# Optimization experiments

Hardware: AMD Instinct MI355X
Metric: run time of the kernel (lower is better)

## Reference

```python
import jax, jax.numpy as jnp
import numpy as np

DIM = 512
HEADS = 8
DIM_HEAD = 64
INNER = HEADS * DIM_HEAD  # 512
HIDDEN = 512 * 4          # mlp_dim * expansion
EPS = 1e-5
SCALE = DIM_HEAD ** -0.5


def layernorm(x, w, b):
    mu = jnp.mean(x, axis=-1, keepdims=True)
    var = jnp.var(x, axis=-1, keepdims=True)
    return (x - mu) * jax.lax.rsqrt(var + EPS) * w + b


def setup_inputs() -> dict:
    key = jax.random.key(0)
    ks = jax.random.split(key, 12)
    B, P, N = 2, 8, 1024  # P must equal HEADS (axis-swap bug in original rearrange)
    s = lambda k, shape, fan: jax.random.normal(k, shape, jnp.float32) * (fan ** -0.5)
    return {
        "x": jax.random.normal(ks[0], (B, P, N, DIM), jnp.float32),
        "ln0_w": jnp.ones((DIM,), jnp.float32),
        "ln0_b": jnp.zeros((DIM,), jnp.float32),
        "ln1_w": jnp.ones((DIM,), jnp.float32),
        "ln1_b": jnp.zeros((DIM,), jnp.float32),
        "w_qkv": s(ks[1], (DIM, 3 * INNER), DIM),
        "w_o": s(ks[2], (INNER, DIM), INNER),
        "b_o": jnp.zeros((DIM,), jnp.float32),
        "w1": s(ks[3], (DIM, HIDDEN), DIM),
        "b1": jnp.zeros((HIDDEN,), jnp.float32),
        "w2": s(ks[4], (HIDDEN, DIM), HIDDEN),
        "b2": jnp.zeros((DIM,), jnp.float32),
    }


def reference(x, ln0_w, ln0_b, ln1_w, ln1_b, w_qkv, w_o, b_o, w1, b1, w2, b2):
    B, P, N, _ = x.shape
    x = layernorm(x, ln0_w, ln0_b)  # outer block norm

    # ---- VisionAttention ----
    h = layernorm(x, ln1_w, ln1_b)
    qkv = h @ w_qkv                                    # [B,P,N,3*INNER]
    q, k, v = jnp.split(qkv, 3, axis=-1)
    def to_heads(t):  # [B,P,N,H*D] -> [B,H,P,N,D]
        return t.reshape(B, P, N, HEADS, DIM_HEAD).transpose(0, 3, 1, 2, 4)
    q, k, v = to_heads(q), to_heads(k), to_heads(v)
    dots = jnp.einsum("bhpnd,bhpmd->bhpnm", q, k) * SCALE  # full NxN scores
    attn = jax.nn.softmax(dots, axis=-1)
    out = jnp.einsum("bhpnm,bhpmd->bhpnd", attn, v)        # [B,H,P,N,D]
    # Faithful to buggy rearrange 'b p h n d -> b p n (h d)': swaps H and P axes.
    out = out.transpose(0, 1, 3, 2, 4).reshape(B, HEADS, N, P * DIM_HEAD)
    out = out @ w_o + b_o                                  # [B,H,N,DIM]
    x = out + x  # residual (valid because P == HEADS)

    # ---- MLP ----
    m = jax.nn.gelu(x @ w1 + b1, approximate=False) @ w2 + b2
    return m + x
```

## Files before the change

### kernel.cpp

```cpp
#include <hip/hip_runtime.h>
#include <hip/hip_bf16.h>
#include <math.h>

#define DIMV 512
#define NTOK 16384
#define NSEQ 1024
#define HEADSV 8
#define PPV 8
#define DHEAD 64
#define QKVW 1536
#define HIDV 2048
#define SC2 0.18033688011112042f

typedef unsigned short ushort;
typedef unsigned int uint;
typedef __attribute__((ext_vector_type(8))) short short8;
typedef __attribute__((ext_vector_type(8))) unsigned short ushort8;
typedef __attribute__((ext_vector_type(4))) unsigned short ushortx4;
typedef __attribute__((ext_vector_type(4))) float floatx4;

__device__ __forceinline__ float bf2f(ushort u){
  union { unsigned int i; float f; } c; c.i = ((unsigned int)u) << 16; return c.f;
}
__device__ __forceinline__ ushort f2bf(float f){
  union { float f; unsigned int i; } c; c.f = f;
  unsigned int u = c.i + 0x7fffu + ((c.i >> 16) & 1u);
  return (ushort)(u >> 16);
}
__device__ __forceinline__ void async_copy16(const void* gptr, void* lptr){
  __builtin_amdgcn_global_load_lds((const __attribute__((address_space(1))) void*)gptr,
                                   (__attribute__((address_space(3))) void*)lptr, 16, 0, 0);
}
__device__ __forceinline__ float fast_gelu(float x){
  float u = x * (2.3022084f + 0.1029435f * x * x);
  return x * __builtin_amdgcn_rcpf(1.f + exp2f(-u));
}

__device__ __forceinline__ void wave_reduce2(float& a, float& b){
  #pragma unroll
  for (int off = 32; off > 0; off >>= 1){
    a += __shfl_down(a, off, 64);
    b += __shfl_down(b, off, 64);
  }
}

__device__ __forceinline__ void wtrans_body(const float* __restrict__ W,
    __hip_bfloat16* __restrict__ Wt, int K, int N, int bx, int by, int t,
    float* tile ){
  int bn = bx * 32, bk = by * 32;
  int tx = t & 31, ty = t >> 5;
  #pragma unroll
  for (int i = 0; i < 32; i += 8)
    tile[(ty + i) * 33 + tx] = W[(size_t)(bk + ty + i) * N + bn + tx];
  __syncthreads();
  #pragma unroll
  for (int i = 0; i < 32; i += 8)
    Wt[(size_t)(bn + ty + i) * K + bk + tx] = __float2bfloat16(tile[tx * 33 + ty + i]);
}

__global__ __launch_bounds__(256) void prep_kernel(const float* __restrict__ x,
    const float* __restrict__ w0, const float* __restrict__ b0,
    const float* __restrict__ w1ln, const float* __restrict__ b1ln,
    __hip_bfloat16* __restrict__ x1, __hip_bfloat16* __restrict__ h,
    const float* __restrict__ wqkv, __hip_bfloat16* __restrict__ wqkvT,
    const float* __restrict__ wo,   __hip_bfloat16* __restrict__ woT,
    const float* __restrict__ w1,   __hip_bfloat16* __restrict__ w1T,
    const float* __restrict__ w2,   __hip_bfloat16* __restrict__ w2T){
  __shared__ float smem[32 * 33];
  int bid = blockIdx.x;
  int t = threadIdx.x;
  if (bid >= NTOK){
    int r = bid - NTOK;
    if (r < 768)        wtrans_body(wqkv, wqkvT, 512, 1536, r % 48, r / 48, t, smem);
    else if (r < 1024){ r -= 768;  wtrans_body(wo, woT, 512, 512,  r % 16, r / 16, t, smem); }
    else if (r < 2048){ r -= 1024; wtrans_body(w1, w1T, 512, 2048, r % 64, r / 64, t, smem); }
    else             { r -= 2048; wtrans_body(w2, w2T, 2048, 512, r % 16, r / 16, t, smem); }
    return;
  }
  float* sm = smem;
  size_t row = bid;
  const float2* xr = (const float2*)(x + row * DIMV);
  float2 v = xr[t];
  float s = v.x + v.y;
  float sq = v.x * v.x + v.y * v.y;
  wave_reduce2(s, sq);
  int wid = t >> 6, lane = t & 63;
  if (lane == 0){ sm[wid] = s; sm[8 + wid] = sq; }
  __syncthreads();
  s  = sm[0] + sm[1] + sm[2] + sm[3];
  sq = sm[8] + sm[9] + sm[10] + sm[11];
  float mu = s * (1.f / DIMV);
  float var = sq * (1.f / DIMV) - mu * mu;
  float r = rsqrtf(var + 1e-5f);
  float2 ww = ((const float2*)w0)[t];
  float2 bb = ((const float2*)b0)[t];
  float2 y;
  y.x = (v.x - mu) * r * ww.x + bb.x;
  y.y = (v.y - mu) * r * ww.y + bb.y;
  ushort2 xb; xb.x = f2bf(y.x); xb.y = f2bf(y.y);
  ((ushort2*)(x1 + row * DIMV))[t] = xb;
  float s2 = y.x + y.y, sq2 = y.x * y.x + y.y * y.y;
  wave_reduce2(s2, sq2);
  __syncthreads();
  if (lane == 0){ sm[wid] = s2; sm[8 + wid] = sq2; }
  __syncthreads();
  s2  = sm[0] + sm[1] + sm[2] + sm[3];
  sq2 = sm[8] + sm[9] + sm[10] + sm[11];
  float mu2 = s2 * (1.f / DIMV);
  float var2 = sq2 * (1.f / DIMV) - mu2 * mu2;
  float r2 = rsqrtf(var2 + 1e-5f);
  float2 w1v = ((const float2*)w1ln)[t];
  float2 b1v = ((const float2*)b1ln)[t];
  float hx = (y.x - mu2) * r2 * w1v.x + b1v.x;
  float hy = (y.y - mu2) * r2 * w1v.y + b1v.y;
  ushort2 hb; hb.x = f2bf(hx); hb.y = f2bf(hy);
  ((ushort2*)(h + row * DIMV))[t] = hb;
}

template<int SWAP>
__global__ __launch_bounds__(256) void gemm_mfma(
    const __hip_bfloat16* __restrict__ A,
    const __hip_bfloat16* __restrict__ Bt,
    const float* __restrict__ bias,
    const __hip_bfloat16* __restrict__ Rb,
    float* __restrict__ Cf,
    __hip_bfloat16* __restrict__ Cb,
    ushort* __restrict__ vt,
    int M, int N, int K, int gx, int dogelu)
{
  __shared__ __hip_bfloat16 As[2][128 * 32];
  __shared__ __hip_bfloat16 Bs[2][128 * 32];
  int tid = threadIdx.x;
  int w = tid >> 6, l = tid & 63;

  int bid = blockIdx.x;
  int xcd = bid & 7, idx = bid >> 3;
  int xl = idx % gx, yl = idx / gx;
  size_t bm = (size_t)(xcd * 16 + yl) * 128;
  size_t bn = (size_t)xl * 128;
  int wm = (w & 1) * 64, wn = (w >> 1) * 64;

  int srow = w * 16 + (l >> 2);
  int scol = (l & 3) * 8;
  const __hip_bfloat16* Ag0 = A + (bm + srow) * K + scol;
  const __hip_bfloat16* Ag1 = A + (bm + 64 + srow) * K + scol;
  const __hip_bfloat16* Bg0 = Bt + (bn + srow) * K + scol;
  const __hip_bfloat16* Bg1 = Bt + (bn + 64 + srow) * K + scol;
  int lo = srow * 32 + scol;

  floatx4 acc[4][4] = {};
  int fm = l & 15;
  int quad = l >> 4;
  int fq = quad * 8;

  async_copy16(Ag0, &As[0][lo]);
  async_copy16(Ag1, &As[0][lo + 64 * 32]);
  async_copy16(Bg0, &Bs[0][lo]);
  async_copy16(Bg1, &Bs[0][lo + 64 * 32]);

  int nk = K >> 5;
  for (int it = 0; it < nk; ++it){
    int cur = it & 1;
    if (it + 1 < nk){
      int nxt = cur ^ 1;
      int k0 = (it + 1) << 5;
      async_copy16(Ag0 + k0, &As[nxt][lo]);
      async_copy16(Ag1 + k0, &As[nxt][lo + 64 * 32]);
      async_copy16(Bg0 + k0, &Bs[nxt][lo]);
      async_copy16(Bg1 + k0, &Bs[nxt][lo + 64 * 32]);
      asm volatile("s_waitcnt vmcnt(4)\n\ts_barrier" ::: "memory");
    } else {
      asm volatile("s_waitcnt vmcnt(0)\n\ts_barrier" ::: "memory");
    }
    const __hip_bfloat16* Ab = As[cur];
    const __hip_bfloat16* Bb = Bs[cur];
    short8 af[4], bf[4];
    #pragma unroll
    for (int i = 0; i < 4; i++){
      af[i] = *(const short8*)&Ab[(wm + i * 16 + fm) * 32 + fq];
      bf[i] = *(const short8*)&Bb[(wn + i * 16 + fm) * 32 + fq];
    }
    #pragma unroll
    for (int mi = 0; mi < 4; mi++)
      #pragma unroll
      for (int ni = 0; ni < 4; ni++){
        if (SWAP)
          acc[mi][ni] = __builtin_amdgcn_mfma_f32_16x16x32_bf16(bf[ni], af[mi], acc[mi][ni], 0, 0, 0);
        else
          acc[mi][ni] = __builtin_amdgcn_mfma_f32_16x16x32_bf16(af[mi], bf[ni], acc[mi][ni], 0, 0, 0);
      }
    asm volatile("s_waitcnt lgkmcnt(0)\n\ts_barrier" ::: "memory");
  }

  int rq = quad * 4;
  if (SWAP){
    #pragma unroll
    for (int mi = 0; mi < 4; mi++){
      size_t row = bm + wm + mi * 16 + fm;
      size_t rbase = row * (size_t)N + bn + wn + rq;
      #pragma unroll
      for (int ni = 0; ni < 4; ni++){
        size_t idx2 = rbase + ni * 16;
        floatx4 v = acc[mi][ni];
        if (bias){
          floatx4 bv = *(const floatx4*)(bias + bn + wn + ni * 16 + rq);
          #pragma unroll
          for (int r2 = 0; r2 < 4; r2++) v[r2] += bv[r2];
        }
        if (dogelu){
          #pragma unroll
          for (int r2 = 0; r2 < 4; r2++) v[r2] = fast_gelu(v[r2]);
        }
        if (Rb){
          ushortx4 rb = *(const ushortx4*)((const ushort*)Rb + idx2);
          #pragma unroll
          for (int r2 = 0; r2 < 4; r2++) v[r2] += bf2f(rb[r2]);
        }
        if (Cb){
          ushortx4 ob;
          #pragma unroll
          for (int r2 = 0; r2 < 4; r2++) ob[r2] = f2bf(v[r2]);
          *(ushortx4*)((ushort*)Cb + idx2) = ob;
        } else {
          *(floatx4*)(Cf + idx2) = v;
        }
      }
    }
  } else {
    if (vt && bn >= 1024){
      int b = (int)(bm >> 13), p = (int)((bm >> 10) & 7);
      int n0 = (int)(bm & 1023) + wm + rq;
      int cbase = (int)bn + wn - 1024;
      #pragma unroll
      for (int ni = 0; ni < 4; ni++){
        int cc = cbase + ni * 16 + fm;
        int hh = cc >> 6, dd = cc & 63;
        ushort* vdst = vt + ((size_t)((b * 8 + hh) * 8 + p)) * 65536 + (size_t)dd * 1024;
        #pragma unroll
        for (int mi = 0; mi < 4; mi++){
          ushortx4 v4;
          v4[0] = f2bf(acc[mi][ni][0]); v4[1] = f2bf(acc[mi][ni][1]);
          v4[2] = f2bf(acc[mi][ni][2]); v4[3] = f2bf(acc[mi][ni][3]);
          *(ushortx4*)(vdst + n0 + mi * 16) = v4;
        }
      }
    } else if (Cb){
      float scl = (vt && bn < 512) ? SC2 : 1.f;
      #pragma unroll
      for (int ni = 0; ni < 4; ni++){
        size_t col = bn + wn + ni * 16 + fm;
        float bv = bias ? bias[col] : 0.f;
        #pragma unroll
        for (int mi = 0; mi < 4; mi++){
          #pragma unroll
          for (int r2 = 0; r2 < 4; r2++){
            size_t row = bm + wm + mi * 16 + rq + r2;
            float v = acc[mi][ni][r2];
            if (vt) v *= scl;
            v += bv;
            if (dogelu) v = fast_gelu(v);
            size_t idx2 = row * N + col;
            if (Rb) v += bf2f(((const ushort*)Rb)[idx2]);
            ((ushort*)Cb)[idx2] = f2bf(v);
          }
        }
      }
    } else {
      #pragma unroll
      for (int ni = 0; ni < 4; ni++){
        size_t col = bn + wn + ni * 16 + fm;
        float bv = bias ? bias[col] : 0.f;
        #pragma unroll
        for (int mi = 0; mi < 4; mi++){
          #pragma unroll
          for (int r2 = 0; r2 < 4; r2++){
            size_t row = bm + wm + mi * 16 + rq + r2;
            float v = acc[mi][ni][r2] + bv;
            if (dogelu) v = fast_gelu(v);
            size_t idx2 = row * N + col;
            if (Rb) v += bf2f(((const ushort*)Rb)[idx2]);
            Cf[idx2] = v;
          }
        }
      }
    }
  }
}

__global__ __launch_bounds__(256, 4) void attn_mfma(const __hip_bfloat16* __restrict__ qkvp,
                                                    const ushort* __restrict__ vt,
                                                    __hip_bfloat16* __restrict__ outp){
  __shared__ ushort Ks[2][64 * 64];
  __shared__ ushort Ps[4][32 * 64];
  int tid = threadIdx.x;
  int w = tid >> 6, l = tid & 63;
  int r15 = l & 15, quad = l >> 4, fq = quad * 8;
  int slice = blockIdx.x & 127;
  int qc = blockIdx.x >> 7;
  int b = slice >> 6, hh = (slice >> 3) & 7, p = slice & 7;
  const ushort* base = (const ushort*)qkvp + (size_t)(b * PPV + p) * NSEQ * QKVW;
  const ushort* kb = base + 512 + hh * DHEAD;
  const ushort* vb = vt + (size_t)slice * 65536;

  int s0 = w * 64 + l, s1 = 256 + w * 64 + l;
  int row0 = s0 >> 3, row1 = s1 >> 3;
  int gc0 = (s0 & 7) ^ (row0 & 7), gc1 = (s1 & 7) ^ (row1 & 7);
  const ushort* kp0 = kb + (size_t)row0 * QKVW + gc0 * 8;
  const ushort* kp1 = kb + (size_t)row1 * QKVW + gc1 * 8;
  ushort* kd0 = &Ks[0][s0 * 8];
  ushort* kd1 = &Ks[0][s1 * 8];

  const ushort* vr[4];
  #pragma unroll
  for (int dj = 0; dj < 4; dj++)
    vr[dj] = vb + (size_t)(dj * 16 + r15) * 1024 + fq;

  int q0 = qc * 128 + w * 32;
  short8 qf[2][2];
  #pragma unroll
  for (int mi = 0; mi < 2; mi++)
    #pragma unroll
    for (int kk = 0; kk < 2; kk++)
      qf[mi][kk] = *(const short8*)(base + (size_t)(q0 + mi * 16 + r15) * QKVW + hh * DHEAD + kk * 32 + fq);

  async_copy16(kp0, kd0);
  async_copy16(kp1, kd1);

  floatx4 o[2][4] = {};
  floatx4 lacc[2] = {};
  short8 ones;
  #pragma unroll
  for (int j = 0; j < 8; j++) ones[j] = (short)0x3F80;

  int sw = r15 & 7;
  int swx = sw << 3;
  ushort* PsW = Ps[w];

  for (int it = 0; it < NSEQ / 64; ++it){
    int cur = it & 1;
    short8 vf[4][2];
    #pragma unroll
    for (int dj = 0; dj < 4; dj++){
      vf[dj][0] = *(const short8*)(vr[dj]);
      vf[dj][1] = *(const short8*)(vr[dj] + 32);
      vr[dj] += 64;
    }
    if (it + 1 < NSEQ / 64){
      int nxt = cur ^ 1;
      kp0 += 64 * QKVW; kp1 += 64 * QKVW;
      async_copy16(kp0, &Ks[nxt][s0 * 8]);
      async_copy16(kp1, &Ks[nxt][s1 * 8]);
      asm volatile("s_waitcnt vmcnt(10)\n\ts_barrier" ::: "memory");
    } else {
      asm volatile("s_waitcnt vmcnt(8)\n\ts_barrier" ::: "memory");
    }
    const ushort* Kb = Ks[cur];

    #pragma unroll
    for (int ni = 0; ni < 4; ni++){
      int rb2 = (ni * 16 + r15) * 64;
      short8 kf0 = *(const short8*)&Kb[rb2 + (quad ^ sw) * 8];
      short8 kf1 = *(const short8*)&Kb[rb2 + ((4 + quad) ^ sw) * 8];
      floatx4 sA = {}, sB = {};
      sA = __builtin_amdgcn_mfma_f32_16x16x32_bf16(kf0, qf[0][0], sA, 0, 0, 0);
      sA = __builtin_amdgcn_mfma_f32_16x16x32_bf16(kf1, qf[0][1], sA, 0, 0, 0);
      sB = __builtin_amdgcn_mfma_f32_16x16x32_bf16(kf0, qf[1][0], sB, 0, 0, 0);
      sB = __builtin_amdgcn_mfma_f32_16x16x32_bf16(kf1, qf[1][1], sB, 0, 0, 0);
      int wc = (ni * 16 + quad * 4) ^ swx;
      #pragma unroll
      for (int mi = 0; mi < 2; mi++){
        const floatx4& sv = mi ? sB : sA;
        union { float f; uint u; } e0, e1, e2, e3;
        e0.f = exp2f(sv[0]);
        e1.f = exp2f(sv[1]);
        e2.f = exp2f(sv[2]);
        e3.f = exp2f(sv[3]);
        uint2 pk;
        pk.x = __builtin_amdgcn_perm(e1.u, e0.u, 0x07060302u);
        pk.y = __builtin_amdgcn_perm(e3.u, e2.u, 0x07060302u);
        *(uint2*)&PsW[(mi * 16 + r15) * 64 + wc] = pk;
      }
    }

    short8 pf[2][2];
    #pragma unroll
    for (int mi = 0; mi < 2; mi++)
      #pragma unroll
      for (int kk = 0; kk < 2; kk++)
        pf[mi][kk] = *(const short8*)&PsW[(mi * 16 + r15) * 64 + ((kk * 32 + fq) ^ swx)];

    #pragma unroll
    for (int mi = 0; mi < 2; mi++)
      #pragma unroll
      for (int kk = 0; kk < 2; kk++)
        lacc[mi] = __builtin_amdgcn_mfma_f32_16x16x32_bf16(ones, pf[mi][kk], lacc[mi], 0, 0, 0);

    #pragma unroll
    for (int dj = 0; dj < 4; dj++){
      #pragma unroll
      for (int mi = 0; mi < 2; mi++){
        o[mi][dj] = __builtin_amdgcn_mfma_f32_16x16x32_bf16(vf[dj][0], pf[mi][0], o[mi][dj], 0, 0, 0);
        o[mi][dj] = __builtin_amdgcn_mfma_f32_16x16x32_bf16(vf[dj][1], pf[mi][1], o[mi][dj], 0, 0, 0);
      }
    }
    asm volatile("s_waitcnt lgkmcnt(0)\n\ts_barrier" ::: "memory");
  }

  #pragma unroll
  for (int mi = 0; mi < 2; mi++){
    float inv = __builtin_amdgcn_rcpf(lacc[mi][0]);
    size_t n = q0 + mi * 16 + r15;
    ushort* orow = (ushort*)outp + ((size_t)((b * HEADSV + hh) * NSEQ + n)) * DIMV + p * DHEAD + quad * 4;
    #pragma unroll
    for (int dj = 0; dj < 4; dj++){
      ushortx4 ov;
      #pragma unroll
      for (int r = 0; r < 4; r++) ov[r] = f2bf(o[mi][dj][r] * inv);
      *(ushortx4*)(orow + dj * 16) = ov;
    }
  }
}

extern "C" void kernel_launch(void* const* d_in, const int* in_sizes, int n_in,
                              void* d_out, int out_size, void* d_ws, size_t ws_size,
                              hipStream_t stream){
  (void)in_sizes; (void)n_in; (void)out_size; (void)ws_size;
  const float* x    = (const float*)d_in[0];
  const float* lw0  = (const float*)d_in[1];
  const float* lb0  = (const float*)d_in[2];
  const float* lw1  = (const float*)d_in[3];
  const float* lb1  = (const float*)d_in[4];
  const float* wqkv = (const float*)d_in[5];
  const float* wo   = (const float*)d_in[6];
  const float* bo   = (const float*)d_in[7];
  const float* w1   = (const float*)d_in[8];
  const float* b1   = (const float*)d_in[9];
  const float* w2   = (const float*)d_in[10];
  const float* b2   = (const float*)d_in[11];
  float* out = (float*)d_out;
  char* ws = (char*)d_ws;
  const size_t MB = 1024 * 1024;

  __hip_bfloat16* x1b  = (__hip_bfloat16*)(ws);
  ushort* vtbuf        = (ushort*)(ws + 32 * MB);
  __hip_bfloat16* x2b  = (__hip_bfloat16*)(ws + 64 * MB);
  __hip_bfloat16* wqkvT= (__hip_bfloat16*)(ws + 80 * MB);
  __hip_bfloat16* woT  = (__hip_bfloat16*)(ws + 82 * MB);
  __hip_bfloat16* w1T  = (__hip_bfloat16*)(ws + 83 * MB);
  __hip_bfloat16* w2T  = (__hip_bfloat16*)(ws + 85 * MB);
  __hip_bfloat16* hB   = (__hip_bfloat16*)(ws + 88 * MB);
  __hip_bfloat16* attnB= hB;
  __hip_bfloat16* qkvB = (__hip_bfloat16*)(ws + 104 * MB);
  __hip_bfloat16* tB   = (__hip_bfloat16*)(ws + 88 * MB);

  prep_kernel<<<NTOK + 3072, 256, 0, stream>>>(
      x, lw0, lb0, lw1, lb1, x1b, hB,
      wqkv, wqkvT, wo, woT, w1, w1T, w2, w2T);

  gemm_mfma<0><<<(QKVW / 128) * 128, 256, 0, stream>>>(
      hB, wqkvT, nullptr, nullptr, nullptr, qkvB, vtbuf,
      NTOK, QKVW, DIMV, QKVW / 128, 0);

  attn_mfma<<<1024, 256, 0, stream>>>(qkvB, vtbuf, attnB);

  gemm_mfma<1><<<(DIMV / 128) * 128, 256, 0, stream>>>(
      attnB, woT, bo, x1b, nullptr, x2b, nullptr,
      NTOK, DIMV, DIMV, DIMV / 128, 0);

  gemm_mfma<1><<<(HIDV / 128) * 128, 256, 0, stream>>>(
      x2b, w1T, b1, nullptr, nullptr, tB, nullptr,
      NTOK, HIDV, DIMV, HIDV / 128, 1);

  gemm_mfma<1><<<(DIMV / 128) * 128, 256, 0, stream>>>(
      tB, w2T, b2, x2b, out, nullptr, nullptr,
      NTOK, DIMV, HIDV, DIMV / 128, 0);
}
```

Measured before the change: 386.8 us.

## Stage V tiles through double-buffered LDS and halve the P scratch buffer

V fragments used to be loaded per thread straight from global memory. They are now copied asynchronously into a double-buffered LDS tile next to K and read back with the swizzled pattern. The score loop is split into two 32-column halves, so each wave's P scratch shrinks to 32x32 and each half is read back before the next one is written. This removes scattered global V loads and cuts P LDS usage, at the cost of more LDS for V and extra lgkmcnt waits inside the loop.

```diff
diff --git a/kernel.cpp b/kernel.cpp
--- a/kernel.cpp
+++ b/kernel.cpp
@@ -291,7 +291,8 @@
                                                     const ushort* __restrict__ vt,
                                                     __hip_bfloat16* __restrict__ outp){
   __shared__ ushort Ks[2][64 * 64];
-  __shared__ ushort Ps[4][32 * 64];
+  __shared__ ushort Vs[2][64 * 64];
+  __shared__ ushort Ps[4][32 * 32];
   int tid = threadIdx.x;
   int w = tid >> 6, l = tid & 63;
   int r15 = l & 15, quad = l >> 4, fq = quad * 8;
@@ -307,13 +308,13 @@
   int gc0 = (s0 & 7) ^ (row0 & 7), gc1 = (s1 & 7) ^ (row1 & 7);
   const ushort* kp0 = kb + (size_t)row0 * QKVW + gc0 * 8;
   const ushort* kp1 = kb + (size_t)row1 * QKVW + gc1 * 8;
-  ushort* kd0 = &Ks[0][s0 * 8];
-  ushort* kd1 = &Ks[0][s1 * 8];
-
-  const ushort* vr[4];
-  #pragma unroll
-  for (int dj = 0; dj < 4; dj++)
-    vr[dj] = vb + (size_t)(dj * 16 + r15) * 1024 + fq;
+  const ushort* vp0 = vb + (size_t)row0 * 1024 + gc0 * 8;
+  const ushort* vp1 = vb + (size_t)row1 * 1024 + gc1 * 8;
+
+  async_copy16(kp0, &Ks[0][s0 * 8]);
+  async_copy16(kp1, &Ks[0][s1 * 8]);
+  async_copy16(vp0, &Vs[0][s0 * 8]);
+  async_copy16(vp1, &Vs[0][s1 * 8]);
 
   int q0 = qc * 128 + w * 32;
   short8 qf[2][2];
@@ -322,9 +323,6 @@
     #pragma unroll
     for (int kk = 0; kk < 2; kk++)
       qf[mi][kk] = *(const short8*)(base + (size_t)(q0 + mi * 16 + r15) * QKVW + hh * DHEAD + kk * 32 + fq);
-
-  async_copy16(kp0, kd0);
-  async_copy16(kp1, kd1);
 
   floatx4 o[2][4] = {};
   floatx4 lacc[2] = {};
@@ -333,61 +331,58 @@
   for (int j = 0; j < 8; j++) ones[j] = (short)0x3F80;
 
   int sw = r15 & 7;
-  int swx = sw << 3;
+  int swp = (r15 & 3) << 3;
   ushort* PsW = Ps[w];
 
   for (int it = 0; it < NSEQ / 64; ++it){
     int cur = it & 1;
-    short8 vf[4][2];
-    #pragma unroll
-    for (int dj = 0; dj < 4; dj++){
-      vf[dj][0] = *(const short8*)(vr[dj]);
-      vf[dj][1] = *(const short8*)(vr[dj] + 32);
-      vr[dj] += 64;
-    }
     if (it + 1 < NSEQ / 64){
       int nxt = cur ^ 1;
-      kp0 += 64 * QKVW; kp1 += 64 * QKVW;
+      kp0 += 64 * QKVW; kp1 += 64 * QKVW; vp0 += 64; vp1 += 64;
       async_copy16(kp0, &Ks[nxt][s0 * 8]);
       async_copy16(kp1, &Ks[nxt][s1 * 8]);
-      asm volatile("s_waitcnt vmcnt(10)\n\ts_barrier" ::: "memory");
+      async_copy16(vp0, &Vs[nxt][s0 * 8]);
+      async_copy16(vp1, &Vs[nxt][s1 * 8]);
+      asm volatile("s_waitcnt vmcnt(4)\n\ts_barrier" ::: "memory");
     } else {
-      asm volatile("s_waitcnt vmcnt(8)\n\ts_barrier" ::: "memory");
+      asm volatile("s_waitcnt vmcnt(0)\n\ts_barrier" ::: "memory");
     }
     const ushort* Kb = Ks[cur];
-
-    #pragma unroll
-    for (int ni = 0; ni < 4; ni++){
-      int rb2 = (ni * 16 + r15) * 64;
-      short8 kf0 = *(const short8*)&Kb[rb2 + (quad ^ sw) * 8];
-      short8 kf1 = *(const short8*)&Kb[rb2 + ((4 + quad) ^ sw) * 8];
-      floatx4 sA = {}, sB = {};
-      sA = __builtin_amdgcn_mfma_f32_16x16x32_bf16(kf0, qf[0][0], sA, 0, 0, 0);
-      sA = __builtin_amdgcn_mfma_f32_16x16x32_bf16(kf1, qf[0][1], sA, 0, 0, 0);
-      sB = __builtin_amdgcn_mfma_f32_16x16x32_bf16(kf0, qf[1][0], sB, 0, 0, 0);
-      sB = __builtin_amdgcn_mfma_f32_16x16x32_bf16(kf1, qf[1][1], sB, 0, 0, 0);
-      int wc = (ni * 16 + quad * 4) ^ swx;
-      #pragma unroll
-      for (int mi = 0; mi < 2; mi++){
-        const floatx4& sv = mi ? sB : sA;
+    const ushort* Vb = Vs[cur];
+
+    short8 pf[2][2];
+    #pragma unroll
+    for (int kk = 0; kk < 2; kk++){
+      #pragma unroll
+      for (int nn = 0; nn < 2; nn++){
+        int ni = kk * 2 + nn;
+        int rb2 = (ni * 16 + r15) * 64;
+        short8 kf0 = *(const short8*)&Kb[rb2 + (quad ^ sw) * 8];
+        short8 kf1 = *(const short8*)&Kb[rb2 + ((4 + quad) ^ sw) * 8];
+        floatx4 sA = {}, sB = {};
+        sA = __builtin_amdgcn_mfma_f32_16x16x32_bf16(kf0, qf[0][0], sA, 0, 0, 0);
+        sA = __builtin_amdgcn_mfma_f32_16x16x32_bf16(kf1, qf[0][1], sA, 0, 0, 0);
+        sB = __builtin_amdgcn_mfma_f32_16x16x32_bf16(kf0, qf[1][0], sB, 0, 0, 0);
+        sB = __builtin_amdgcn_mfma_f32_16x16x32_bf16(kf1, qf[1][1], sB, 0, 0, 0);
+        int wc = (nn * 16 + quad * 4) ^ swp;
         union { float f; uint u; } e0, e1, e2, e3;
-        e0.f = exp2f(sv[0]);
-        e1.f = exp2f(sv[1]);
-        e2.f = exp2f(sv[2]);
-        e3.f = exp2f(sv[3]);
         uint2 pk;
+        e0.f = exp2f(sA[0]); e1.f = exp2f(sA[1]);
+        e2.f = exp2f(sA[2]); e3.f = exp2f(sA[3]);
         pk.x = __builtin_amdgcn_perm(e1.u, e0.u, 0x07060302u);
         pk.y = __builtin_amdgcn_perm(e3.u, e2.u, 0x07060302u);
-        *(uint2*)&PsW[(mi * 16 + r15) * 64 + wc] = pk;
-      }
-    }
-
-    short8 pf[2][2];
-    #pragma unroll
-    for (int mi = 0; mi < 2; mi++)
-      #pragma unroll
-      for (int kk = 0; kk < 2; kk++)
-        pf[mi][kk] = *(const short8*)&PsW[(mi * 16 + r15) * 64 + ((kk * 32 + fq) ^ swx)];
+        *(uint2*)&PsW[r15 * 32 + wc] = pk;
+        e0.f = exp2f(sB[0]); e1.f = exp2f(sB[1]);
+        e2.f = exp2f(sB[2]); e3.f = exp2f(sB[3]);
+        pk.x = __builtin_amdgcn_perm(e1.u, e0.u, 0x07060302u);
+        pk.y = __builtin_amdgcn_perm(e3.u, e2.u, 0x07060302u);
+        *(uint2*)&PsW[(16 + r15) * 32 + wc] = pk;
+      }
+      asm volatile("s_waitcnt lgkmcnt(0)" ::: "memory");
+      pf[0][kk] = *(const short8*)&PsW[r15 * 32 + (fq ^ swp)];
+      pf[1][kk] = *(const short8*)&PsW[(16 + r15) * 32 + (fq ^ swp)];
+      asm volatile("s_waitcnt lgkmcnt(0)" ::: "memory");
+    }
 
     #pragma unroll
     for (int mi = 0; mi < 2; mi++)
@@ -397,10 +392,13 @@
 
     #pragma unroll
     for (int dj = 0; dj < 4; dj++){
+      int d = dj * 16 + r15;
+      short8 vf0 = *(const short8*)&Vb[d * 64 + ((quad) ^ sw) * 8];
+      short8 vf1 = *(const short8*)&Vb[d * 64 + ((4 + quad) ^ sw) * 8];
       #pragma unroll
       for (int mi = 0; mi < 2; mi++){
-        o[mi][dj] = __builtin_amdgcn_mfma_f32_16x16x32_bf16(vf[dj][0], pf[mi][0], o[mi][dj], 0, 0, 0);
-        o[mi][dj] = __builtin_amdgcn_mfma_f32_16x16x32_bf16(vf[dj][1], pf[mi][1], o[mi][dj], 0, 0, 0);
+        o[mi][dj] = __builtin_amdgcn_mfma_f32_16x16x32_bf16(vf0, pf[mi][0], o[mi][dj], 0, 0, 0);
+        o[mi][dj] = __builtin_amdgcn_mfma_f32_16x16x32_bf16(vf1, pf[mi][1], o[mi][dj], 0, 0, 0);
       }
     }
     asm volatile("s_waitcnt lgkmcnt(0)\n\ts_barrier" ::: "memory");
```

New measurement: 372.7 us. 3.6% less time.
